# Optimization experiments

Measured on AMD Instinct MI355X. Metric: run time of the kernel, lower is better.

## Reference

```python
import jax, jax.numpy as jnp
import numpy as np

B, D, H = 256, 512, 256
K = 5
MARGIN = 1.0
TAU = 1.0
LAM_C = 0.01
LAM_E = 0.1
BETA = 0.1
LN_EPS = 1e-5


def _layernorm(x, g, b):
    mu = jnp.mean(x, axis=-1, keepdims=True)
    var = jnp.var(x, axis=-1, keepdims=True)
    return (x - mu) * jax.lax.rsqrt(var + LN_EPS) * g + b


def setup_inputs() -> dict:
    key = jax.random.key(0)
    ks = jax.random.split(key, 16)
    s = 0.02
    inp = {
        "outputs": jax.random.normal(ks[0], (B, 3, 64, 64), jnp.float32),
        "images": jax.random.normal(ks[1], (B, 3, 64, 64), jnp.float32),
        "f_orig": jax.random.normal(ks[2], (B, D), jnp.float32),
        "f_recon": jax.random.normal(ks[3], (B, D), jnp.float32),
        "cf1": jax.random.normal(ks[4], (B, 256, 8, 8), jnp.float32),
        "cf2": jax.random.normal(ks[5], (B, 512, 4, 4), jnp.float32),
        # EnergyNet encoder params
        "W1": jax.random.normal(ks[6], (D, H), jnp.float32) * s,
        "b1": jnp.zeros((H,), jnp.float32),
        "g1": jnp.ones((H,), jnp.float32),
        "be1": jnp.zeros((H,), jnp.float32),
        "W2": jax.random.normal(ks[7], (H, H), jnp.float32) * s,
        "b2": jnp.zeros((H,), jnp.float32),
        # EnergyNet interaction params
        "W3": jax.random.normal(ks[8], (3 * H, H), jnp.float32) * s,
        "b3": jnp.zeros((H,), jnp.float32),
        "g3": jnp.ones((H,), jnp.float32),
        "be3": jnp.zeros((H,), jnp.float32),
        "W4": jax.random.normal(ks[9], (H, H // 2), jnp.float32) * s,
        "b4": jnp.zeros((H // 2,), jnp.float32),
        "W5": jax.random.normal(ks[10], (H // 2, 1), jnp.float32) * s,
        "b5": jnp.zeros((1,), jnp.float32),
    }
    return inp


def _encoder(x, W1, b1, g1, be1, W2, b2):
    h = _layernorm(x @ W1 + b1, g1, be1)
    return jax.nn.relu(h) @ W2 + b2


def _energy_matrix(f1, f2, W1, b1, g1, be1, W2, b2, W3, b3, g3, be3, W4, b4, W5, b5):
    e1 = _encoder(f1, W1, b1, g1, be1, W2, b2)  # [B,H]
    e2 = _encoder(f2, W1, b1, g1, be1, W2, b2)  # [B,H]
    e1b = jnp.broadcast_to(e1[:, None, :], (B, B, H))
    e2b = jnp.broadcast_to(e2[None, :, :], (B, B, H))
    combined = jnp.concatenate([e1b, e2b, e1b * e2b], axis=-1)  # [B,B,3H]
    h = jax.nn.relu(_layernorm(combined @ W3 + b3, g3, be3))
    h = jax.nn.relu(h @ W4 + b4)
    return (h @ W5 + b5)[..., 0]  # [B,B]


def _topk_neighbors(f, k):
    fn = f / (jnp.linalg.norm(f, axis=1, keepdims=True))
    sim = fn @ fn.T
    sim = jnp.where(jnp.eye(f.shape[0], dtype=bool), -jnp.inf, sim)
    _, idx = jax.lax.top_k(sim, k)  # [B,k]
    onehot = jnp.zeros((f.shape[0], f.shape[0]), jnp.float32)
    rows = jnp.arange(f.shape[0])[:, None]
    return onehot.at[rows, idx].set(1.0)


def _entropy(x):
    xn = (x - x.min()) / (x.max() - x.min() + 1e-8)
    # torch.histc(bins=256, min=0, max=1): values at max go to last bin
    idx = jnp.clip(jnp.floor(xn.reshape(-1) * 256.0).astype(jnp.int32), 0, 255)
    hist = jnp.bincount(idx, length=256).astype(jnp.float32)
    p = hist / hist.sum()
    return -jnp.sum(p * jnp.log2(p + 1e-8))


def reference(outputs, images, f_orig, f_recon, cf1, cf2,
              W1, b1, g1, be1, W2, b2, W3, b3, g3, be3, W4, b4, W5, b5):
    # reconstruction loss
    recon = jnp.mean((outputs - images) ** 2)

    # energy margin loss
    E = _energy_matrix(f_orig, f_recon, W1, b1, g1, be1, W2, b2,
                       W3, b3, g3, be3, W4, b4, W5, b5)
    pos = jnp.diag(E)[:, None]
    losses = jax.nn.relu(MARGIN + E - pos)
    neg_mask = ~jnp.eye(B, dtype=bool)
    standard_loss = jnp.sum(losses * neg_mask) / (B * (B - 1))

    k = min(K, B - 1)
    on = _topk_neighbors(f_orig, k)
    rn = _topk_neighbors(f_recon, k)
    inter = jnp.sum(on * rn, axis=1)
    union = jnp.sum(jnp.clip(on + rn, 0.0, 1.0), axis=1)
    jaccard = inter / (union + 1e-8)
    neighbor_loss = 1.0 - jnp.mean(jaccard)
    energy_loss = standard_loss + 0.3 * neighbor_loss

    # compression loss over the dict of compressed features {cf1, cf2}
    sp = 0.5 * (jnp.mean(jnp.abs(cf1)) + jnp.mean(jnp.abs(cf2)))
    en = 0.5 * (_entropy(cf1) + _entropy(cf2))
    compress = sp + BETA * en

    total = recon + LAM_C * compress + LAM_E * energy_loss
    return (total, recon, energy_loss, compress)
```

## Files before the change

kernel.cpp:

```cpp
#include <hip/hip_runtime.h>
#include <math.h>

typedef __attribute__((ext_vector_type(8))) short short8;
typedef __attribute__((ext_vector_type(4))) float f32x4;
typedef __attribute__((ext_vector_type(4))) unsigned int u32x4;

union U8 { unsigned int u[4]; short8 s; u32x4 v; };


__device__ __forceinline__ float wave_sum(float v) {
#pragma unroll
    for (int o = 32; o > 0; o >>= 1) v += __shfl_down(v, o);
    return v;
}

__device__ __forceinline__ float block_sum256(float v, float* red) {
    v = wave_sum(v);
    int t = threadIdx.x;
    if ((t & 63) == 0) red[t >> 6] = v;
    __syncthreads();
    float r = red[0] + red[1] + red[2] + red[3];
    __syncthreads();
    return r;
}

__device__ __forceinline__ unsigned fenc(float f) {
    unsigned u = __float_as_uint(f);
    return (u & 0x80000000u) ? ~u : (u | 0x80000000u);
}
__device__ __forceinline__ float fdec(unsigned u) {
    return (u & 0x80000000u) ? __uint_as_float(u & 0x7fffffffu) : __uint_as_float(~u);
}

__device__ __forceinline__ ushort f2bf(float f) {
    unsigned u = __float_as_uint(f);
    unsigned r = (u + 0x7fffu + ((u >> 16) & 1u)) >> 16;
    return (ushort)r;
}
__device__ __forceinline__ float bflo(unsigned u) { return __uint_as_float(u << 16); }
__device__ __forceinline__ float bfhi(unsigned u) { return __uint_as_float(u & 0xffff0000u); }
__device__ __forceinline__ float bf2f(ushort u) { return __uint_as_float((unsigned)u << 16); }


__global__ void init_kernel(float* wsf, unsigned* wsu, int* wsi) {
    int t = threadIdx.x;
    if (t < 7) wsf[t] = 0.f;
    if (t == 7 || t == 9) wsu[t] = 0xFFFFFFFFu;
    if (t == 8 || t == 10) wsu[t] = 0u;
    wsi[16 + t] = 0;
    wsi[272 + t] = 0;
}

__device__ __forceinline__ void pack256(const float* __restrict__ src, ushort* __restrict__ dst, int s) {
    int lane = s & 63;
    int tt = (s >> 6) & 15;
    int kk = s >> 10;
    int qq = lane >> 4, nn = lane & 15;
    int tcol = tt * 16 + nn;
    short8 v;
#pragma unroll
    for (int jj = 0; jj < 8; ++jj) {
        int k = kk * 32 + qq * 8 + jj;
        v[jj] = (short)f2bf(src[(size_t)k * 256 + tcol]);
    }
    *(short8*)(dst + (size_t)s * 8) = v;
}

__device__ __forceinline__ void pack128(const float* __restrict__ src, ushort* __restrict__ dst, int s) {
    int lane = s & 63;
    int tt = (s >> 6) & 7;
    int kk = s >> 9;
    int qq = lane >> 4, nn = lane & 15;
    int ncol = tt * 16 + nn;
    short8 v;
#pragma unroll
    for (int jj = 0; jj < 8; ++jj) {
        int k = kk * 32 + qq * 8 + jj;
        v[jj] = (short)f2bf(src[(size_t)k * 128 + ncol]);
    }
    *(short8*)(dst + (size_t)s * 8) = v;
}

__global__ __launch_bounds__(256) void mega_kernel(
    const float4* __restrict__ o, const float4* __restrict__ im,
    const float4* __restrict__ cf1, const float4* __restrict__ cf2,
    const float* __restrict__ fo, const float* __restrict__ fr,
    const float* __restrict__ W1, const float* __restrict__ W2,
    const float* __restrict__ W3, const float* __restrict__ W4,
    float* wsf, unsigned* wsu, float* rnorm, float* fT,
    ushort* __restrict__ W3cpk, ushort* __restrict__ W4pk,
    ushort* __restrict__ W1pk, ushort* __restrict__ W2pk,
    ushort* __restrict__ W3apk, ushort* __restrict__ W3bpk) {
    __shared__ float smem[64 * 33];
    float* red = smem;
    int b = blockIdx.x, t = threadIdx.x;
    if (b < 2048) {
        if (b < 512) {
            int base = b * 1536 + t;
            float4 av[6], cv[6];
#pragma unroll
            for (int u = 0; u < 6; ++u) { av[u] = o[base + u * 256]; cv[u] = im[base + u * 256]; }
            float s0 = 0.f, s1 = 0.f;
#pragma unroll
            for (int u = 0; u < 6; ++u) {
                float dx = av[u].x - cv[u].x, dy = av[u].y - cv[u].y;
                float dz = av[u].z - cv[u].z, dw = av[u].w - cv[u].w;
                if (u & 1) s1 += dx * dx + dy * dy + dz * dz + dw * dw;
                else s0 += dx * dx + dy * dy + dz * dz + dw * dw;
            }
            float tot = block_sum256(s0 + s1, red);
            if (t == 0) atomicAdd(wsf + 0, tot);
        } else if (b < 1536) {
            int which = (b < 1024) ? 0 : 1;
            const float4* x = which ? cf2 : cf1;
            int niter = which ? 4 : 8;
            int base = which ? ((b - 1024) * 1024 + t) : ((b - 512) * 2048 + t);
            float4 v[8];
            for (int u = 0; u < niter; ++u) v[u] = x[base + u * 256];
            float s = 0.f, mn = INFINITY, mx = -INFINITY;
            for (int u = 0; u < niter; ++u) {
                float4 a = v[u];
                s += fabsf(a.x) + fabsf(a.y) + fabsf(a.z) + fabsf(a.w);
                mn = fminf(mn, fminf(fminf(a.x, a.y), fminf(a.z, a.w)));
                mx = fmaxf(mx, fmaxf(fmaxf(a.x, a.y), fmaxf(a.z, a.w)));
            }
            float tot = block_sum256(s, red);
#pragma unroll
            for (int off = 32; off > 0; off >>= 1) {
                mn = fminf(mn, __shfl_down(mn, off));
                mx = fmaxf(mx, __shfl_down(mx, off));
            }
            float* rmn = smem + 8;
            float* rmx = smem + 16;
            if ((t & 63) == 0) { rmn[t >> 6] = mn; rmx[t >> 6] = mx; }
            __syncthreads();
            if (t == 0) {
                atomicAdd(wsf + 1 + which, tot);
                float m1 = fminf(fminf(rmn[0], rmn[1]), fminf(rmn[2], rmn[3]));
                float m2 = fmaxf(fmaxf(rmx[0], rmx[1]), fmaxf(rmx[2], rmx[3]));
                atomicMin(wsu + 7 + which * 2, fenc(m1));
                atomicMax(wsu + 8 + which * 2, fenc(m2));
            }
        } else {
            int r = b - 1536;
            const float4* f = (r < 256) ? ((const float4*)fo + (size_t)r * 128)
                                        : ((const float4*)fr + (size_t)(r - 256) * 128);
            float s = 0.f;
            if (t < 128) {
                float4 a = f[t];
                s = a.x * a.x + a.y * a.y + a.z * a.z + a.w * a.w;
            }
            float tot = block_sum256(s, red);
            if (t == 0) rnorm[r] = 1.0f / sqrtf(tot);
        }
    } else if (b < 2176) {
        int bb = b - 2048;
        int pass = bb >> 6;
        int kt = (bb >> 2) & 15;
        int jt = bb & 3;
        int k0 = kt * 32, j0 = jt * 64;
        const float* f = pass ? fr : fo;
        float (*tile)[33] = (float(*)[33])smem;
        int cl = t & 31, rl = t >> 5;
#pragma unroll
        for (int r = 0; r < 8; ++r) {
            int row = j0 + rl + r * 8;
            tile[rl + r * 8][cl] = f[(size_t)row * 512 + k0 + cl];
        }
        __syncthreads();
        int jl = t & 63, kq = t >> 6;
        float* dst = fT + (size_t)pass * 131072;
#pragma unroll
        for (int c = 0; c < 8; ++c) {
            int kl = kq * 8 + c;
            dst[(size_t)(k0 + kl) * 256 + j0 + jl] = tile[jl][kl];
        }
    } else {
        int pb = b - 2176;
        if (pb < 32) pack256(W3 + 512 * 256, W3cpk, pb * 256 + t);
        else if (pb < 48) pack128(W4, W4pk, (pb - 32) * 256 + t);
        else if (pb < 112) pack256(W1, W1pk, (pb - 48) * 256 + t);
        else if (pb < 144) pack256(W2, W2pk, (pb - 112) * 256 + t);
        else if (pb < 176) pack256(W3, W3apk, (pb - 144) * 256 + t);
        else pack256(W3 + 256 * 256, W3bpk, (pb - 176) * 256 + t);
    }
}

__global__ __launch_bounds__(256) void hist_kernel(const float4* __restrict__ cf1,
                                                   const float4* __restrict__ cf2,
                                                   const unsigned* wsu, int* wsi) {
    __shared__ int hl[256];
    int b = blockIdx.x, t = threadIdx.x;
    hl[t] = 0;
    __syncthreads();
    int which = (b < 512) ? 0 : 1;
    const float4* x = which ? cf2 : cf1;
    int niter = which ? 4 : 8;
    int base = which ? ((b - 512) * 1024 + t) : (b * 2048 + t);
    int* hist = wsi + (which ? 272 : 16);
    float mn = fdec(wsu[7 + which * 2]), mx = fdec(wsu[8 + which * 2]);
    float inv = 256.f / (mx - mn + 1e-8f);
    float4 v[8];
    for (int u = 0; u < niter; ++u) v[u] = x[base + u * 256];
    for (int u = 0; u < niter; ++u) {
        float4 a = v[u];
        int b0i = min(max((int)floorf((a.x - mn) * inv), 0), 255);
        int b1i = min(max((int)floorf((a.y - mn) * inv), 0), 255);
        int b2i = min(max((int)floorf((a.z - mn) * inv), 0), 255);
        int b3i = min(max((int)floorf((a.w - mn) * inv), 0), 255);
        atomicAdd(&hl[b0i], 1);
        atomicAdd(&hl[b1i], 1);
        atomicAdd(&hl[b2i], 1);
        atomicAdd(&hl[b3i], 1);
    }
    __syncthreads();
    if (hl[t]) atomicAdd(&hist[t], hl[t]);
}

__global__ __launch_bounds__(256) void encoder_mfma(
    const float* __restrict__ fo, const float* __restrict__ fr,
    const ushort* __restrict__ W1p, const ushort* __restrict__ W2p,
    const ushort* __restrict__ W3ap, const ushort* __restrict__ W3bp,
    const float* __restrict__ b1, const float* __restrict__ g1,
    const float* __restrict__ be1, const float* __restrict__ b2,
    ushort* __restrict__ ebf, ushort* __restrict__ A1bf, ushort* __restrict__ A2bf)
{
    int blk = blockIdx.x;
    int t = threadIdx.x;
    int w = t >> 6, lane = t & 63, q = lane >> 4, n = lane & 15;
    int r = blk * 64 + w * 16 + n;
    bool isOrig = (r < 256);
    const float* f = isOrig ? (fo + (size_t)r * 512) : (fr + (size_t)(r - 256) * 512);

    f32x4 acc[16];
#pragma unroll
    for (int tt = 0; tt < 16; ++tt) acc[tt] = (f32x4){0.f, 0.f, 0.f, 0.f};
    for (int kk = 0; kk < 16; ++kk) {
        int kb = kk * 32 + q * 8;
        float4 fa = *(const float4*)(f + kb);
        float4 fb = *(const float4*)(f + kb + 4);
        U8 bb;
        bb.u[0] = (unsigned)f2bf(fa.x) | ((unsigned)f2bf(fa.y) << 16);
        bb.u[1] = (unsigned)f2bf(fa.z) | ((unsigned)f2bf(fa.w) << 16);
        bb.u[2] = (unsigned)f2bf(fb.x) | ((unsigned)f2bf(fb.y) << 16);
        bb.u[3] = (unsigned)f2bf(fb.z) | ((unsigned)f2bf(fb.w) << 16);
        const ushort* wp = W1p + ((size_t)(kk * 1024 + lane)) * 8;
#pragma unroll
        for (int tt = 0; tt < 16; ++tt) {
            short8 af = *(const short8*)(wp + (size_t)tt * 512);
            acc[tt] = __builtin_amdgcn_mfma_f32_16x16x32_bf16(af, bb.s, acc[tt], 0, 0, 0);
        }
    }
    float s1 = 0.f, s2 = 0.f;
#pragma unroll
    for (int tt = 0; tt < 16; ++tt) {
        int tb = tt * 16 + q * 4;
        float4 bv = *(const float4*)(b1 + tb);
        float v0 = acc[tt][0] + bv.x, v1 = acc[tt][1] + bv.y;
        float v2 = acc[tt][2] + bv.z, v3 = acc[tt][3] + bv.w;
        acc[tt][0] = v0; acc[tt][1] = v1; acc[tt][2] = v2; acc[tt][3] = v3;
        s1 += v0 + v1 + v2 + v3;
        s2 += v0 * v0 + v1 * v1 + v2 * v2 + v3 * v3;
    }
    s1 += __shfl_xor(s1, 16); s1 += __shfl_xor(s1, 32);
    s2 += __shfl_xor(s2, 16); s2 += __shfl_xor(s2, 32);
    float mean = s1 * (1.f / 256.f);
    float var = s2 * (1.f / 256.f) - mean * mean;
    float rstd = rsqrtf(var + 1e-5f);
    uint2 pk[16];
#pragma unroll
    for (int tt = 0; tt < 16; ++tt) {
        int tb = tt * 16 + q * 4;
        float4 gg = *(const float4*)(g1 + tb);
        float4 be = *(const float4*)(be1 + tb);
        float h0 = fmaxf((acc[tt][0] - mean) * rstd * gg.x + be.x, 0.f);
        float h1 = fmaxf((acc[tt][1] - mean) * rstd * gg.y + be.y, 0.f);
        float h2 = fmaxf((acc[tt][2] - mean) * rstd * gg.z + be.z, 0.f);
        float h3 = fmaxf((acc[tt][3] - mean) * rstd * gg.w + be.w, 0.f);
        pk[tt].x = (unsigned)f2bf(h0) | ((unsigned)f2bf(h1) << 16);
        pk[tt].y = (unsigned)f2bf(h2) | ((unsigned)f2bf(h3) << 16);
    }

    int qh = (q >> 1) & 1;
    int src0 = ((q & 1) * 2) * 16 + n;
    int src1 = src0 + 16;

    f32x4 eacc[16];
#pragma unroll
    for (int tt = 0; tt < 16; ++tt) eacc[tt] = (f32x4){0.f, 0.f, 0.f, 0.f};
#pragma unroll
    for (int kk = 0; kk < 8; ++kk) {
        uint2 lo2 = pk[kk * 2], hi2 = pk[kk * 2 + 1];
        unsigned a0 = (unsigned)__shfl((int)lo2.x, src0);
        unsigned a1 = (unsigned)__shfl((int)lo2.y, src0);
        unsigned b0 = (unsigned)__shfl((int)hi2.x, src0);
        unsigned b1v = (unsigned)__shfl((int)hi2.y, src0);
        unsigned c0 = (unsigned)__shfl((int)lo2.x, src1);
        unsigned c1 = (unsigned)__shfl((int)lo2.y, src1);
        unsigned d0 = (unsigned)__shfl((int)hi2.x, src1);
        unsigned d1 = (unsigned)__shfl((int)hi2.y, src1);
        U8 hb;
        hb.u[0] = qh ? b0 : a0;
        hb.u[1] = qh ? b1v : a1;
        hb.u[2] = qh ? d0 : c0;
        hb.u[3] = qh ? d1 : c1;
        const ushort* wp = W2p + ((size_t)(kk * 1024 + lane)) * 8;
#pragma unroll
        for (int tt = 0; tt < 16; ++tt) {
            short8 af = *(const short8*)(wp + (size_t)tt * 512);
            eacc[tt] = __builtin_amdgcn_mfma_f32_16x16x32_bf16(af, hb.s, eacc[tt], 0, 0, 0);
        }
    }
    uint2 epk[16];
#pragma unroll
    for (int tt = 0; tt < 16; ++tt) {
        int tb = tt * 16 + q * 4;
        float4 bv = *(const float4*)(b2 + tb);
        float e0 = eacc[tt][0] + bv.x, e1 = eacc[tt][1] + bv.y;
        float e2 = eacc[tt][2] + bv.z, e3 = eacc[tt][3] + bv.w;
        epk[tt].x = (unsigned)f2bf(e0) | ((unsigned)f2bf(e1) << 16);
        epk[tt].y = (unsigned)f2bf(e2) | ((unsigned)f2bf(e3) << 16);
        *(uint2*)(ebf + (size_t)r * 256 + tb) = epk[tt];
    }

    const ushort* W3x = isOrig ? W3ap : W3bp;
    f32x4 aacc[16];
#pragma unroll
    for (int tt = 0; tt < 16; ++tt) aacc[tt] = (f32x4){0.f, 0.f, 0.f, 0.f};
#pragma unroll
    for (int kk = 0; kk < 8; ++kk) {
        uint2 lo2 = epk[kk * 2], hi2 = epk[kk * 2 + 1];
        unsigned a0 = (unsigned)__shfl((int)lo2.x, src0);
        unsigned a1 = (unsigned)__shfl((int)lo2.y, src0);
        unsigned b0 = (unsigned)__shfl((int)hi2.x, src0);
        unsigned b1v = (unsigned)__shfl((int)hi2.y, src0);
        unsigned c0 = (unsigned)__shfl((int)lo2.x, src1);
        unsigned c1 = (unsigned)__shfl((int)lo2.y, src1);
        unsigned d0 = (unsigned)__shfl((int)hi2.x, src1);
        unsigned d1 = (unsigned)__shfl((int)hi2.y, src1);
        U8 hb;
        hb.u[0] = qh ? b0 : a0;
        hb.u[1] = qh ? b1v : a1;
        hb.u[2] = qh ? d0 : c0;
        hb.u[3] = qh ? d1 : c1;
        const ushort* wp = W3x + ((size_t)(kk * 1024 + lane)) * 8;
#pragma unroll
        for (int tt = 0; tt < 16; ++tt) {
            short8 af = *(const short8*)(wp + (size_t)tt * 512);
            aacc[tt] = __builtin_amdgcn_mfma_f32_16x16x32_bf16(af, hb.s, aacc[tt], 0, 0, 0);
        }
    }
    ushort* dst = isOrig ? (A1bf + (size_t)r * 256) : (A2bf + (size_t)(r - 256) * 256);
#pragma unroll
    for (int tt = 0; tt < 16; ++tt) {
        int tb = tt * 16 + q * 4;
        uint2 pv;
        pv.x = (unsigned)f2bf(aacc[tt][0]) | ((unsigned)f2bf(aacc[tt][1]) << 16);
        pv.y = (unsigned)f2bf(aacc[tt][2]) | ((unsigned)f2bf(aacc[tt][3]) << 16);
        *(uint2*)(dst + tb) = pv;
    }
}

__global__ __launch_bounds__(256) void simtop_kernel(const float* __restrict__ fo,
                                                     const float* __restrict__ fr,
                                                     const float* __restrict__ rnorm,
                                                     const float* __restrict__ fT,
                                                     int* __restrict__ top5) {
    int b = blockIdx.x;
    int pass = b >> 7, pair = b & 127;
    int i0 = pair * 2, i1 = i0 + 1;
    const float* f = pass ? fr : fo;
    const float* rn = rnorm + pass * 256;
    __shared__ float2 fs2[512];
    __shared__ float candV[4][2][5];
    __shared__ int candI[4][2][5];
    int t = threadIdx.x;
    const float* f0 = f + (size_t)i0 * 512;
    const float* f1 = f + (size_t)i1 * 512;
    fs2[t] = make_float2(f0[t], f1[t]);
    fs2[t + 256] = make_float2(f0[t + 256], f1[t + 256]);
    __syncthreads();
    int j = t;
    const float* col = fT + (size_t)pass * 131072 + j;
    float x0 = 0.f, x1 = 0.f, y0 = 0.f, y1 = 0.f, z0 = 0.f, z1 = 0.f, u0 = 0.f, u1 = 0.f;
#pragma unroll 8
    for (int k = 0; k < 128; ++k) {
        float v0 = col[(size_t)k * 256];
        float v1 = col[(size_t)(k + 128) * 256];
        float v2 = col[(size_t)(k + 256) * 256];
        float v3 = col[(size_t)(k + 384) * 256];
        float2 g0 = fs2[k], g1 = fs2[k + 128], g2 = fs2[k + 256], g3 = fs2[k + 384];
        x0 += g0.x * v0; x1 += g0.y * v0;
        y0 += g1.x * v1; y1 += g1.y * v1;
        z0 += g2.x * v2; z1 += g2.y * v2;
        u0 += g3.x * v3; u1 += g3.y * v3;
    }
    float a0 = ((x0 + y0) + (z0 + u0)) * rn[j];
    float a1 = ((x1 + y1) + (z1 + u1)) * rn[j];
    if (j == i0) a0 = -INFINITY;
    if (j == i1) a1 = -INFINITY;
    int w = t >> 6, lane = t & 63;
    for (int sel = 0; sel < 2; ++sel) {
        float v2 = sel ? a1 : a0;
        int idx = j;
        for (int r = 0; r < 5; ++r) {
            float m = v2;
            int mi = idx;
#pragma unroll
            for (int off = 32; off > 0; off >>= 1) {
                float om = __shfl_xor(m, off);
                int omi = __shfl_xor(mi, off);
                if (om > m || (om == m && omi < mi)) { m = om; mi = omi; }
            }
            if (lane == 0) { candV[w][sel][r] = m; candI[w][sel][r] = mi; }
            if (idx == mi) v2 = -INFINITY;
        }
    }
    __syncthreads();
    if (w < 2) {
        float v = -INFINITY;
        int ix = 0x7fffffff;
        if (lane < 20) { v = candV[lane / 5][w][lane % 5]; ix = candI[lane / 5][w][lane % 5]; }
        int iSel = w ? i1 : i0;
        for (int r = 0; r < 5; ++r) {
            float m = v;
            int mi = ix;
#pragma unroll
            for (int off = 32; off > 0; off >>= 1) {
                float om = __shfl_xor(m, off);
                int omi = __shfl_xor(mi, off);
                if (om > m || (om == m && omi < mi)) { m = om; mi = omi; }
            }
            if (lane == 0) top5[((size_t)pass * 256 + iSel) * 5 + r] = mi;
            if (ix == mi) v = -INFINITY;
        }
    }
}

__global__ __launch_bounds__(256, 2) void energy_v4(
    const ushort* __restrict__ A1bf, const ushort* __restrict__ A2bf,
    const ushort* __restrict__ ebf,
    const ushort* __restrict__ W3p, const ushort* __restrict__ W4p,
    const float* __restrict__ b3, const float* __restrict__ g3, const float* __restrict__ be3,
    const float* __restrict__ b4, const float* __restrict__ W5, const float* __restrict__ b5,
    ushort* __restrict__ E)
{
    int blk = blockIdx.x;
    int i = blk >> 1;
    int half = blk & 1;
    int t = threadIdx.x;
    int w = t >> 6, lane = t & 63, q = lane >> 4, n = lane & 15;
    int jb = half * 128 + w * 32;
    __shared__ float combS[256], g3S[256], be3S[256], b4S[128], w5S[128];
    combS[t] = bf2f(A1bf[(size_t)i * 256 + t]) + b3[t];
    g3S[t] = g3[t];
    be3S[t] = be3[t];
    if (t < 128) { b4S[t] = b4[t]; w5S[t] = W5[t]; }
    __syncthreads();

    const ushort* e1p = ebf + (size_t)i * 256;
    const ushort* e2p = ebf + 65536;

    f32x4 acc[2][16];
#pragma unroll
    for (int s = 0; s < 2; ++s)
#pragma unroll
        for (int tt = 0; tt < 16; ++tt) acc[s][tt] = (f32x4){0.f, 0.f, 0.f, 0.f};

    for (int kk = 0; kk < 8; ++kk) {
        int kbase = kk * 32 + q * 8;
        U8 e1v;
        e1v.v = *(const u32x4*)(e1p + kbase);
        float e1f[8];
#pragma unroll
        for (int x = 0; x < 4; ++x) {
            e1f[2 * x] = bflo(e1v.u[x]);
            e1f[2 * x + 1] = bfhi(e1v.u[x]);
        }
        short8 bfrag[2];
#pragma unroll
        for (int s = 0; s < 2; ++s) {
            U8 e2v;
            e2v.v = *(const u32x4*)(e2p + (size_t)(jb + s * 16 + n) * 256 + kbase);
            U8 bb;
#pragma unroll
            for (int x = 0; x < 4; ++x) {
                float p0 = bflo(e2v.u[x]) * e1f[2 * x];
                float p1 = bfhi(e2v.u[x]) * e1f[2 * x + 1];
                bb.u[x] = (unsigned)f2bf(p0) | ((unsigned)f2bf(p1) << 16);
            }
            bfrag[s] = bb.s;
        }
        const ushort* wp = W3p + ((size_t)(kk * 16) * 64 + lane) * 8;
#pragma unroll
        for (int tt = 0; tt < 16; ++tt) {
            short8 af = *(const short8*)(wp + (size_t)tt * 512);
            acc[0][tt] = __builtin_amdgcn_mfma_f32_16x16x32_bf16(af, bfrag[0], acc[0][tt], 0, 0, 0);
            acc[1][tt] = __builtin_amdgcn_mfma_f32_16x16x32_bf16(af, bfrag[1], acc[1][tt], 0, 0, 0);
        }
    }

    uint2 pk[2][16];
    float b5v = b5[0];
#pragma unroll
    for (int s = 0; s < 2; ++s) {
        int j = jb + s * 16 + n;
        float s1 = 0.f, s2 = 0.f;
#pragma unroll
        for (int tt = 0; tt < 16; ++tt) {
            int tb = tt * 16 + q * 4;
            float4 cb = *(const float4*)(combS + tb);
            uint2 a2u = *(const uint2*)(A2bf + (size_t)j * 256 + tb);
            float a0 = bflo(a2u.x), a1f = bfhi(a2u.x), a2f = bflo(a2u.y), a3f = bfhi(a2u.y);
            float v0 = acc[s][tt][0] + cb.x + a0;
            float v1 = acc[s][tt][1] + cb.y + a1f;
            float v2 = acc[s][tt][2] + cb.z + a2f;
            float v3 = acc[s][tt][3] + cb.w + a3f;
            acc[s][tt][0] = v0; acc[s][tt][1] = v1; acc[s][tt][2] = v2; acc[s][tt][3] = v3;
            s1 += v0 + v1 + v2 + v3;
            s2 += v0 * v0 + v1 * v1 + v2 * v2 + v3 * v3;
        }
        s1 += __shfl_xor(s1, 16); s1 += __shfl_xor(s1, 32);
        s2 += __shfl_xor(s2, 16); s2 += __shfl_xor(s2, 32);
        float mean = s1 * (1.f / 256.f);
        float var = s2 * (1.f / 256.f) - mean * mean;
        float rstd = rsqrtf(var + 1e-5f);
#pragma unroll
        for (int tt = 0; tt < 16; ++tt) {
            int tb = tt * 16 + q * 4;
            float4 gg = *(const float4*)(g3S + tb);
            float4 be = *(const float4*)(be3S + tb);
            float h0 = fmaxf((acc[s][tt][0] - mean) * rstd * gg.x + be.x, 0.f);
            float h1 = fmaxf((acc[s][tt][1] - mean) * rstd * gg.y + be.y, 0.f);
            float h2 = fmaxf((acc[s][tt][2] - mean) * rstd * gg.z + be.z, 0.f);
            float h3 = fmaxf((acc[s][tt][3] - mean) * rstd * gg.w + be.w, 0.f);
            pk[s][tt].x = (unsigned)f2bf(h0) | ((unsigned)f2bf(h1) << 16);
            pk[s][tt].y = (unsigned)f2bf(h2) | ((unsigned)f2bf(h3) << 16);
        }
    }

    f32x4 gacc[2][8];
#pragma unroll
    for (int s = 0; s < 2; ++s)
#pragma unroll
        for (int nt = 0; nt < 8; ++nt) gacc[s][nt] = (f32x4){0.f, 0.f, 0.f, 0.f};

    int qh = (q >> 1) & 1;
    int src0 = ((q & 1) * 2) * 16 + n;
    int src1 = src0 + 16;
#pragma unroll
    for (int kk = 0; kk < 8; ++kk) {
        const ushort* wp = W4p + ((size_t)(kk * 8) * 64 + lane) * 8;
#pragma unroll
        for (int s = 0; s < 2; ++s) {
            uint2 lo2 = pk[s][kk * 2], hi2 = pk[s][kk * 2 + 1];
            unsigned a0 = (unsigned)__shfl((int)lo2.x, src0);
            unsigned a1 = (unsigned)__shfl((int)lo2.y, src0);
            unsigned b0 = (unsigned)__shfl((int)hi2.x, src0);
            unsigned b1 = (unsigned)__shfl((int)hi2.y, src0);
            unsigned c0 = (unsigned)__shfl((int)lo2.x, src1);
            unsigned c1 = (unsigned)__shfl((int)lo2.y, src1);
            unsigned d0 = (unsigned)__shfl((int)hi2.x, src1);
            unsigned d1 = (unsigned)__shfl((int)hi2.y, src1);
            U8 hb;
            hb.u[0] = qh ? b0 : a0;
            hb.u[1] = qh ? b1 : a1;
            hb.u[2] = qh ? d0 : c0;
            hb.u[3] = qh ? d1 : c1;
#pragma unroll
            for (int nt = 0; nt < 8; ++nt) {
                short8 wa = *(const short8*)(wp + (size_t)nt * 512);
                gacc[s][nt] = __builtin_amdgcn_mfma_f32_16x16x32_bf16(wa, hb.s, gacc[s][nt], 0, 0, 0);
            }
        }
    }

#pragma unroll
    for (int s = 0; s < 2; ++s) {
        float ep = 0.f;
#pragma unroll
        for (int nt = 0; nt < 8; ++nt) {
            int nb = nt * 16 + q * 4;
            float4 b4v = *(const float4*)(b4S + nb);
            float4 w5v = *(const float4*)(w5S + nb);
            ep += fmaxf(gacc[s][nt][0] + b4v.x, 0.f) * w5v.x;
            ep += fmaxf(gacc[s][nt][1] + b4v.y, 0.f) * w5v.y;
            ep += fmaxf(gacc[s][nt][2] + b4v.z, 0.f) * w5v.z;
            ep += fmaxf(gacc[s][nt][3] + b4v.w, 0.f) * w5v.w;
        }
        ep += __shfl_xor(ep, 16);
        ep += __shfl_xor(ep, 32);
        if (q == 0) E[(size_t)i * 256 + jb + s * 16 + n] = f2bf(ep + b5v);
    }
}

__global__ void margin_jac_kernel(const ushort* __restrict__ E, const int* __restrict__ top5,
                                  float* slAcc, float* jacOut) {
    __shared__ float red[4];
    int b = blockIdx.x, t = threadIdx.x;
    if (b < 256) {
        float diag = bf2f(E[(size_t)b * 256 + b]);
        float l = (t == b) ? 0.f : fmaxf(1.f + bf2f(E[(size_t)b * 256 + t]) - diag, 0.f);
        float tot = block_sum256(l, red);
        if (t == 0) atomicAdd(slAcc, tot);
    } else {
        int O[5], R[5];
#pragma unroll
        for (int r = 0; r < 5; ++r) {
            O[r] = top5[t * 5 + r];
            R[r] = top5[(256 + t) * 5 + r];
        }
        int inter = 0;
#pragma unroll
        for (int a = 0; a < 5; ++a)
#pragma unroll
            for (int bq = 0; bq < 5; ++bq) inter += (O[a] == R[bq]);
        float fi2 = (float)inter;
        float jac = fi2 / (10.f - fi2 + 1e-8f);
        float s = block_sum256(jac, red);
        if (t == 0) jacOut[0] = s;
    }
}

__global__ void finalize_kernel(const float* wsf, const int* h1, const int* h2, float* out) {
    __shared__ float red[4];
    int t = threadIdx.x;
    float p1 = (float)h1[t] / 4194304.f;
    float p2 = (float)h2[t] / 2097152.f;
    float s1 = block_sum256(-p1 * log2f(p1 + 1e-8f), red);
    float s2 = block_sum256(-p2 * log2f(p2 + 1e-8f), red);
    if (t == 0) {
        float recon = wsf[0] / 3145728.f;
        float sp = 0.5f * (wsf[1] / 4194304.f + wsf[2] / 2097152.f);
        float en = 0.5f * (s1 + s2);
        float compress = sp + 0.1f * en;
        float sl = wsf[5] / (256.f * 255.f);
        float nl = 1.f - wsf[6] / 256.f;
        float energy = sl + 0.3f * nl;
        float total = recon + 0.01f * compress + 0.1f * energy;
        out[0] = total;
        out[1] = recon;
        out[2] = energy;
        out[3] = compress;
    }
}

extern "C" void kernel_launch(void* const* d_in, const int* in_sizes, int n_in,
                              void* d_out, int out_size, void* d_ws, size_t ws_size,
                              hipStream_t stream) {
    const float* outputs = (const float*)d_in[0];
    const float* images  = (const float*)d_in[1];
    const float* f_orig  = (const float*)d_in[2];
    const float* f_recon = (const float*)d_in[3];
    const float* cf1 = (const float*)d_in[4];
    const float* cf2 = (const float*)d_in[5];
    const float* W1 = (const float*)d_in[6];
    const float* b1 = (const float*)d_in[7];
    const float* g1 = (const float*)d_in[8];
    const float* be1 = (const float*)d_in[9];
    const float* W2 = (const float*)d_in[10];
    const float* b2 = (const float*)d_in[11];
    const float* W3 = (const float*)d_in[12];
    const float* b3 = (const float*)d_in[13];
    const float* g3 = (const float*)d_in[14];
    const float* be3 = (const float*)d_in[15];
    const float* W4 = (const float*)d_in[16];
    const float* b4 = (const float*)d_in[17];
    const float* W5 = (const float*)d_in[18];
    const float* b5 = (const float*)d_in[19];

    float* wsf = (float*)d_ws;
    unsigned* wsu = (unsigned*)d_ws;
    int* wsi = (int*)d_ws;
    float* out = (float*)d_out;

    float* rnorm = wsf + 528;
    ushort* A1bf = (ushort*)(wsf + 1040);
    ushort* A2bf = (ushort*)(wsf + 33808);
    ushort* ebf  = (ushort*)(wsf + 66576);
    ushort* Ebf  = (ushort*)(wsf + 132112);
    ushort* W3cpk = (ushort*)(wsf + 164880);
    ushort* W4pk  = (ushort*)(wsf + 197648);
    ushort* W1pk  = (ushort*)(wsf + 214032);
    ushort* W2pk  = (ushort*)(wsf + 279568);
    ushort* W3apk = (ushort*)(wsf + 312336);
    ushort* W3bpk = (ushort*)(wsf + 345104);
    float* fT = wsf + 377872;
    int* top5 = wsi + 640016;

    hipLaunchKernelGGL(init_kernel, dim3(1), dim3(256), 0, stream, wsf, wsu, wsi);
    hipLaunchKernelGGL(mega_kernel, dim3(2384), dim3(256), 0, stream,
                       (const float4*)outputs, (const float4*)images,
                       (const float4*)cf1, (const float4*)cf2,
                       f_orig, f_recon, W1, W2, W3, W4,
                       wsf, wsu, rnorm, fT, W3cpk, W4pk, W1pk, W2pk, W3apk, W3bpk);
    hipLaunchKernelGGL(hist_kernel, dim3(1024), dim3(256), 0, stream,
                       (const float4*)cf1, (const float4*)cf2, wsu, wsi);
    hipLaunchKernelGGL(encoder_mfma, dim3(8), dim3(256), 0, stream,
                       f_orig, f_recon, W1pk, W2pk, W3apk, W3bpk,
                       b1, g1, be1, b2, ebf, A1bf, A2bf);
    hipLaunchKernelGGL(simtop_kernel, dim3(256), dim3(256), 0, stream,
                       f_orig, f_recon, rnorm, fT, top5);
    hipLaunchKernelGGL(energy_v4, dim3(512), dim3(256), 0, stream,
                       A1bf, A2bf, ebf, W3cpk, W4pk, b3, g3, be3, b4, W5, b5, Ebf);
    hipLaunchKernelGGL(margin_jac_kernel, dim3(257), dim3(256), 0, stream,
                       Ebf, top5, wsf + 5, wsf + 6);
    hipLaunchKernelGGL(finalize_kernel, dim3(1), dim3(256), 0, stream,
                       wsf, wsi + 16, wsi + 272, out);
}
```

Baseline: 343.1 us.

## Split encoder into single-wave blocks and double-buffer MFMA weight fragments in registers

The encoder kernel now launches 32 one-wave blocks instead of 8 four-wave blocks, so the 32 waves can spread across more compute units. Each K-step's weight fragments are prefetched into a second register buffer while the current step's MFMAs run, to hide global-load latency. The cost is much higher register pressure (two 16-fragment buffers on top of 16 accumulators), which may cause spills. Every wave still re-reads all the weights, so total weight traffic stays the same.

```diff
diff --git a/kernel.cpp b/kernel.cpp
--- a/kernel.cpp
+++ b/kernel.cpp
@@ -217,7 +217,7 @@
     if (hl[t]) atomicAdd(&hist[t], hl[t]);
 }
 
-__global__ __launch_bounds__(256) void encoder_mfma(
+__global__ __launch_bounds__(64, 1) void encoder_mfma(
     const float* __restrict__ fo, const float* __restrict__ fr,
     const ushort* __restrict__ W1p, const ushort* __restrict__ W2p,
     const ushort* __restrict__ W3ap, const ushort* __restrict__ W3bp,
@@ -225,17 +225,30 @@
     const float* __restrict__ be1, const float* __restrict__ b2,
     ushort* __restrict__ ebf, ushort* __restrict__ A1bf, ushort* __restrict__ A2bf)
 {
-    int blk = blockIdx.x;
-    int t = threadIdx.x;
-    int w = t >> 6, lane = t & 63, q = lane >> 4, n = lane & 15;
-    int r = blk * 64 + w * 16 + n;
+    int lane = threadIdx.x & 63;
+    int q = lane >> 4, n = lane & 15;
+    int r = blockIdx.x * 16 + n;
     bool isOrig = (r < 256);
     const float* f = isOrig ? (fo + (size_t)r * 512) : (fr + (size_t)(r - 256) * 512);
 
     f32x4 acc[16];
 #pragma unroll
     for (int tt = 0; tt < 16; ++tt) acc[tt] = (f32x4){0.f, 0.f, 0.f, 0.f};
+    short8 wA[16], wB[16];
+    {
+        const ushort* wp0 = W1p + (size_t)lane * 8;
+#pragma unroll
+        for (int tt = 0; tt < 16; ++tt) wA[tt] = *(const short8*)(wp0 + (size_t)tt * 512);
+    }
+#pragma unroll
     for (int kk = 0; kk < 16; ++kk) {
+        const short8* cur = (kk & 1) ? wB : wA;
+        short8* nxt = (kk & 1) ? wA : wB;
+        if (kk < 15) {
+            const ushort* wpn = W1p + ((size_t)((kk + 1) * 1024 + lane)) * 8;
+#pragma unroll
+            for (int tt = 0; tt < 16; ++tt) nxt[tt] = *(const short8*)(wpn + (size_t)tt * 512);
+        }
         int kb = kk * 32 + q * 8;
         float4 fa = *(const float4*)(f + kb);
         float4 fb = *(const float4*)(f + kb + 4);
@@ -244,12 +257,9 @@
         bb.u[1] = (unsigned)f2bf(fa.z) | ((unsigned)f2bf(fa.w) << 16);
         bb.u[2] = (unsigned)f2bf(fb.x) | ((unsigned)f2bf(fb.y) << 16);
         bb.u[3] = (unsigned)f2bf(fb.z) | ((unsigned)f2bf(fb.w) << 16);
-        const ushort* wp = W1p + ((size_t)(kk * 1024 + lane)) * 8;
-#pragma unroll
-        for (int tt = 0; tt < 16; ++tt) {
-            short8 af = *(const short8*)(wp + (size_t)tt * 512);
-            acc[tt] = __builtin_amdgcn_mfma_f32_16x16x32_bf16(af, bb.s, acc[tt], 0, 0, 0);
-        }
+#pragma unroll
+        for (int tt = 0; tt < 16; ++tt)
+            acc[tt] = __builtin_amdgcn_mfma_f32_16x16x32_bf16(cur[tt], bb.s, acc[tt], 0, 0, 0);
     }
     float s1 = 0.f, s2 = 0.f;
 #pragma unroll
@@ -288,8 +298,20 @@
     f32x4 eacc[16];
 #pragma unroll
     for (int tt = 0; tt < 16; ++tt) eacc[tt] = (f32x4){0.f, 0.f, 0.f, 0.f};
+    {
+        const ushort* wp0 = W2p + (size_t)lane * 8;
+#pragma unroll
+        for (int tt = 0; tt < 16; ++tt) wA[tt] = *(const short8*)(wp0 + (size_t)tt * 512);
+    }
 #pragma unroll
     for (int kk = 0; kk < 8; ++kk) {
+        const short8* cur = (kk & 1) ? wB : wA;
+        short8* nxt = (kk & 1) ? wA : wB;
+        if (kk < 7) {
+            const ushort* wpn = W2p + ((size_t)((kk + 1) * 1024 + lane)) * 8;
+#pragma unroll
+            for (int tt = 0; tt < 16; ++tt) nxt[tt] = *(const short8*)(wpn + (size_t)tt * 512);
+        }
         uint2 lo2 = pk[kk * 2], hi2 = pk[kk * 2 + 1];
         unsigned a0 = (unsigned)__shfl((int)lo2.x, src0);
         unsigned a1 = (unsigned)__shfl((int)lo2.y, src0);
@@ -304,12 +326,9 @@
         hb.u[1] = qh ? b1v : a1;
         hb.u[2] = qh ? d0 : c0;
         hb.u[3] = qh ? d1 : c1;
-        const ushort* wp = W2p + ((size_t)(kk * 1024 + lane)) * 8;
-#pragma unroll
-        for (int tt = 0; tt < 16; ++tt) {
-            short8 af = *(const short8*)(wp + (size_t)tt * 512);
-            eacc[tt] = __builtin_amdgcn_mfma_f32_16x16x32_bf16(af, hb.s, eacc[tt], 0, 0, 0);
-        }
+#pragma unroll
+        for (int tt = 0; tt < 16; ++tt)
+            eacc[tt] = __builtin_amdgcn_mfma_f32_16x16x32_bf16(cur[tt], hb.s, eacc[tt], 0, 0, 0);
     }
     uint2 epk[16];
 #pragma unroll
@@ -327,8 +346,20 @@
     f32x4 aacc[16];
 #pragma unroll
     for (int tt = 0; tt < 16; ++tt) aacc[tt] = (f32x4){0.f, 0.f, 0.f, 0.f};
+    {
+        const ushort* wp0 = W3x + (size_t)lane * 8;
+#pragma unroll
+        for (int tt = 0; tt < 16; ++tt) wA[tt] = *(const short8*)(wp0 + (size_t)tt * 512);
+    }
 #pragma unroll
     for (int kk = 0; kk < 8; ++kk) {
+        const short8* cur = (kk & 1) ? wB : wA;
+        short8* nxt = (kk & 1) ? wA : wB;
+        if (kk < 7) {
+            const ushort* wpn = W3x + ((size_t)((kk + 1) * 1024 + lane)) * 8;
+#pragma unroll
+            for (int tt = 0; tt < 16; ++tt) nxt[tt] = *(const short8*)(wpn + (size_t)tt * 512);
+        }
         uint2 lo2 = epk[kk * 2], hi2 = epk[kk * 2 + 1];
         unsigned a0 = (unsigned)__shfl((int)lo2.x, src0);
         unsigned a1 = (unsigned)__shfl((int)lo2.y, src0);
@@ -343,12 +374,9 @@
         hb.u[1] = qh ? b1v : a1;
         hb.u[2] = qh ? d0 : c0;
         hb.u[3] = qh ? d1 : c1;
-        const ushort* wp = W3x + ((size_t)(kk * 1024 + lane)) * 8;
-#pragma unroll
-        for (int tt = 0; tt < 16; ++tt) {
-            short8 af = *(const short8*)(wp + (size_t)tt * 512);
-            aacc[tt] = __builtin_amdgcn_mfma_f32_16x16x32_bf16(af, hb.s, aacc[tt], 0, 0, 0);
-        }
+#pragma unroll
+        for (int tt = 0; tt < 16; ++tt)
+            aacc[tt] = __builtin_amdgcn_mfma_f32_16x16x32_bf16(cur[tt], hb.s, aacc[tt], 0, 0, 0);
     }
     ushort* dst = isOrig ? (A1bf + (size_t)r * 256) : (A2bf + (size_t)(r - 256) * 256);
 #pragma unroll
@@ -696,7 +724,7 @@
                        wsf, wsu, rnorm, fT, W3cpk, W4pk, W1pk, W2pk, W3apk, W3bpk);
     hipLaunchKernelGGL(hist_kernel, dim3(1024), dim3(256), 0, stream,
                        (const float4*)cf1, (const float4*)cf2, wsu, wsi);
-    hipLaunchKernelGGL(encoder_mfma, dim3(8), dim3(256), 0, stream,
+    hipLaunchKernelGGL(encoder_mfma, dim3(32), dim3(64), 0, stream,
                        f_orig, f_recon, W1pk, W2pk, W3apk, W3bpk,
                        b1, g1, be1, b2, ebf, A1bf, A2bf);
     hipLaunchKernelGGL(simtop_kernel, dim3(256), dim3(256), 0, stream,
```

New measurement: 277.8 us. -19.0%, faster.
